# Kernel optimization log

Measured on AMD Instinct MI355X. Metric: run time of the kernel, lower is better.

Reference implementation:

```python
import jax, jax.numpy as jnp
import numpy as np

N_NODES = 100000
N_EDGES = 600000
D = 128


def setup_inputs() -> dict:
    key = jax.random.key(0)
    k_h, k_ei, k_ea, k_wm, k_bm, k_wu, k_bu = jax.random.split(key, 7)
    h = jax.random.normal(k_h, (N_NODES, D), dtype=jnp.float32)
    edge_index = jax.random.randint(k_ei, (2, N_EDGES), 0, N_NODES, dtype=jnp.int64)
    edge_attr = jax.random.normal(k_ea, (N_EDGES, D), dtype=jnp.float32)
    # nn.Linear params (W stored as [out, in] in torch; keep [in, out] here)
    s_m = 1.0 / np.sqrt(3 * D)
    s_u = 1.0 / np.sqrt(2 * D)
    W_msg = jax.random.uniform(k_wm, (3 * D, D), jnp.float32, -s_m, s_m)
    b_msg = jax.random.uniform(k_bm, (D,), jnp.float32, -s_m, s_m)
    W_upd = jax.random.uniform(k_wu, (2 * D, D), jnp.float32, -s_u, s_u)
    b_upd = jax.random.uniform(k_bu, (D,), jnp.float32, -s_u, s_u)
    return {"h": h, "edge_index": edge_index, "edge_attr": edge_attr,
            "W_msg": W_msg, "b_msg": b_msg, "W_upd": W_upd, "b_upd": b_upd}


def reference(h, edge_index, edge_attr, W_msg, b_msg, W_upd, b_upd):
    send, rec = edge_index[0], edge_index[1]
    h_send = h[send]                      # [E, D] gather
    h_rec = h[rec]                        # [E, D] gather
    msg_in = jnp.concatenate((h_send, h_rec, edge_attr), axis=1)  # [E, 3D]
    messages = msg_in @ W_msg + b_msg     # [E, D]
    messages_agg = jax.ops.segment_sum(messages, rec, num_segments=h.shape[0])  # [N, D]
    upd_in = jnp.concatenate((h, messages_agg), axis=1)           # [N, 2D]
    out = upd_in @ W_upd + b_upd          # [N, D]
    return out
```

## Files before the change

### kernel.cpp

```cpp
#include <hip/hip_runtime.h>

#define N_NODES 100000
#define N_EDGES 600000
#define D 128
#define MAXDEG 64
#define OVF_CAP 4096

typedef __attribute__((ext_vector_type(8))) short bf16x8;
typedef __attribute__((ext_vector_type(4))) float f32x4;

static __device__ inline ushort f2bf(float f) {
    unsigned x = __float_as_uint(f);
    unsigned r = (x + 0x7fffu + ((x >> 16) & 1u)) >> 16;
    return (ushort)r;
}


__global__ void k_zero(int* __restrict__ cnt) {
    int i = blockIdx.x * 256 + threadIdx.x;
    if (i < N_NODES + 1) cnt[i] = 0;
}

__global__ void k_build_w(const float* __restrict__ W_msg,
                          const float* __restrict__ b_msg,
                          const float* __restrict__ W_upd,
                          ushort* __restrict__ Wfrag,
                          float* __restrict__ Wcat32,
                          float* __restrict__ bv)
{
    int gid = blockIdx.x * 256 + threadIdx.x;
    if (gid < 512 * 128) {
        int i = gid & 7;
        int l = (gid >> 3) & 63;
        int fb = gid >> 9;
        int kb = fb >> 3, cb = fb & 7;
        int k = kb * 32 + ((l >> 4) * 8) + i;
        int j = cb * 16 + (l & 15);
        float acc;
        if (k < 128) {
            acc = W_upd[k * 128 + j];
        } else {
            int r = k - 128;
            acc = 0.f;
            #pragma unroll 4
            for (int dd = 0; dd < 128; ++dd)
                acc += W_msg[r * 128 + dd] * W_upd[(128 + dd) * 128 + j];
        }
        Wfrag[gid] = f2bf(acc);
        Wcat32[k * 128 + j] = acc;
    } else if (gid < 512 * 128 + 128) {
        int j = gid - 512 * 128;
        float acc = 0.f;
        for (int dd = 0; dd < 128; ++dd)
            acc += b_msg[dd] * W_upd[(128 + dd) * 128 + j];
        bv[j] = acc;
    }
}

__global__ void k_bucket(const int* __restrict__ eidx,
                         int* __restrict__ cnt,
                         int* __restrict__ ovf,
                         int2* __restrict__ elist2)
{
    int e = blockIdx.x * 256 + threadIdx.x;
    if (e >= N_EDGES) return;
    int s = eidx[e];
    int r = eidx[N_EDGES + e];
    int slot = atomicAdd(cnt + r, 1);
    if (slot < MAXDEG) {
        elist2[(size_t)r * MAXDEG + slot] = make_int2(e, s);
    } else {
        int p = atomicAdd(cnt + N_NODES, 1);
        if (p < OVF_CAP) ovf[p] = e;
    }
}

__global__ __launch_bounds__(256, 4) void k_fused(
    const float* __restrict__ h,
    const float* __restrict__ ea,
    const int* __restrict__ cnt,
    const int2* __restrict__ elist2,
    const ushort* __restrict__ Wfrag,
    const float* __restrict__ bv,
    const float* __restrict__ b_upd,
    float* __restrict__ out)
{
    __shared__ ushort Xs[32][520];
    __shared__ float degL[32];
    const int tid = threadIdx.x;
    const int lane = tid & 63;
    const int wv = tid >> 6;
    const int n0 = blockIdx.x * 32;

    for (int u = 0; u < 8; ++u) {
        const int i = wv * 8 + u;
        const int n = n0 + i;
        const int c = cnt[n];
        const int m = c < MAXDEG ? c : MAXDEG;
        const float2 hn = *(const float2*)(h + (size_t)n * D + lane * 2);
        int2 es = make_int2(0, 0);
        if (lane < m) es = elist2[(size_t)n * MAXDEG + lane];

        float Sx = 0.f, Sy = 0.f, Ex = 0.f, Ey = 0.f;
        int t = 0;
        for (; t + 4 <= m; t += 4) {
            int e0 = __shfl(es.x, t + 0), s0 = __shfl(es.y, t + 0);
            int e1 = __shfl(es.x, t + 1), s1 = __shfl(es.y, t + 1);
            int e2 = __shfl(es.x, t + 2), s2 = __shfl(es.y, t + 2);
            int e3 = __shfl(es.x, t + 3), s3 = __shfl(es.y, t + 3);
            float2 a0 = *(const float2*)(h  + (size_t)s0 * D + lane * 2);
            float2 a1 = *(const float2*)(h  + (size_t)s1 * D + lane * 2);
            float2 a2 = *(const float2*)(h  + (size_t)s2 * D + lane * 2);
            float2 a3 = *(const float2*)(h  + (size_t)s3 * D + lane * 2);
            float2 b0 = *(const float2*)(ea + (size_t)e0 * D + lane * 2);
            float2 b1 = *(const float2*)(ea + (size_t)e1 * D + lane * 2);
            float2 b2 = *(const float2*)(ea + (size_t)e2 * D + lane * 2);
            float2 b3 = *(const float2*)(ea + (size_t)e3 * D + lane * 2);
            Sx += (a0.x + a1.x) + (a2.x + a3.x);
            Sy += (a0.y + a1.y) + (a2.y + a3.y);
            Ex += (b0.x + b1.x) + (b2.x + b3.x);
            Ey += (b0.y + b1.y) + (b2.y + b3.y);
        }
        for (; t < m; ++t) {
            int e = __shfl(es.x, t), s = __shfl(es.y, t);
            float2 a = *(const float2*)(h  + (size_t)s * D + lane * 2);
            float2 b = *(const float2*)(ea + (size_t)e * D + lane * 2);
            Sx += a.x; Sy += a.y; Ex += b.x; Ey += b.y;
        }
        const float dv = (float)c;
        ushort2 q;
        q.x = f2bf(hn.x);      q.y = f2bf(hn.y);
        *(ushort2*)&Xs[i][      lane * 2] = q;
        q.x = f2bf(Sx);        q.y = f2bf(Sy);
        *(ushort2*)&Xs[i][128 + lane * 2] = q;
        q.x = f2bf(dv * hn.x); q.y = f2bf(dv * hn.y);
        *(ushort2*)&Xs[i][256 + lane * 2] = q;
        q.x = f2bf(Ex);        q.y = f2bf(Ey);
        *(ushort2*)&Xs[i][384 + lane * 2] = q;
        if (lane == 0) degL[i] = dv;
    }
    __syncthreads();

    const int rb = wv >> 1;
    const int cbg = wv & 1;
    const int arow = rb * 16 + (lane & 15);
    const int koff = (lane >> 4) * 8;

    f32x4 acc[4] = {};
    for (int kb = 0; kb < 16; ++kb) {
        bf16x8 a = *(const bf16x8*)&Xs[arow][kb * 32 + koff];
        #pragma unroll
        for (int cc = 0; cc < 4; ++cc) {
            int fb = kb * 8 + cbg * 4 + cc;
            bf16x8 b = *(const bf16x8*)(Wfrag + ((size_t)fb * 64 + lane) * 8);
            acc[cc] = __builtin_amdgcn_mfma_f32_16x16x32_bf16(a, b, acc[cc], 0, 0, 0);
        }
    }

    const int r0 = (lane >> 4) * 4;
    #pragma unroll
    for (int cc = 0; cc < 4; ++cc) {
        int col = cbg * 64 + cc * 16 + (lane & 15);
        float bvv = bv[col];
        float buv = b_upd[col];
        #pragma unroll
        for (int r = 0; r < 4; ++r) {
            int rl = rb * 16 + r0 + r;
            out[(size_t)(n0 + rl) * D + col] = acc[cc][r] + degL[rl] * bvv + buv;
        }
    }
}

__global__ void k_ovf(const float* __restrict__ h,
                      const int* __restrict__ eidx,
                      const float* __restrict__ ea,
                      const int* __restrict__ cnt,
                      const int* __restrict__ ovf,
                      const float* __restrict__ Wcat32,
                      float* __restrict__ out)
{
    int ncnt = cnt[N_NODES];
    if (ncnt > OVF_CAP) ncnt = OVF_CAP;
    if (ncnt <= 0) return;
    int lane = threadIdx.x & 63;
    int w = threadIdx.x >> 6;
    for (int i = w; i < ncnt; i += 4) {
        int e = ovf[i];
        int s = eidx[e];
        int r = eidx[N_EDGES + e];
        float acc0 = 0.f, acc1 = 0.f;
        for (int dd = 0; dd < 128; ++dd) {
            float hs = h[(size_t)s * D + dd];
            float ev = ea[(size_t)e * D + dd];
            acc0 += hs * Wcat32[(128 + dd) * 128 + lane * 2]     + ev * Wcat32[(384 + dd) * 128 + lane * 2];
            acc1 += hs * Wcat32[(128 + dd) * 128 + lane * 2 + 1] + ev * Wcat32[(384 + dd) * 128 + lane * 2 + 1];
        }
        atomicAdd(out + (size_t)r * D + lane * 2 + 0, acc0);
        atomicAdd(out + (size_t)r * D + lane * 2 + 1, acc1);
    }
}

extern "C" void kernel_launch(void* const* d_in, const int* in_sizes, int n_in,
                              void* d_out, int out_size, void* d_ws, size_t ws_size,
                              hipStream_t stream)
{
    const float* h     = (const float*)d_in[0];
    const int*   eidx  = (const int*)d_in[1];
    const float* eattr = (const float*)d_in[2];
    const float* W_msg = (const float*)d_in[3];
    const float* b_msg = (const float*)d_in[4];
    const float* W_upd = (const float*)d_in[5];
    const float* b_upd = (const float*)d_in[6];
    float* out = (float*)d_out;

    ushort* Wfrag  = (ushort*)d_ws;
    float*  Wcat32 = (float*)((char*)d_ws + 131072);
    float*  bv     = Wcat32 + 512 * 128;
    int*    cnt    = (int*)(bv + 128);
    int*    ovf    = cnt + 100002;
    int2*   elist2 = (int2*)(ovf + OVF_CAP);

    k_zero<<<(N_NODES + 1 + 255) / 256, 256, 0, stream>>>(cnt);
    k_build_w<<<(512 * 128 + 128 + 255) / 256, 256, 0, stream>>>(W_msg, b_msg, W_upd, Wfrag, Wcat32, bv);
    k_bucket<<<(N_EDGES + 255) / 256, 256, 0, stream>>>(eidx, cnt, ovf, elist2);
    k_fused<<<N_NODES / 32, 256, 0, stream>>>(h, eattr, cnt, elist2, Wfrag, bv, b_upd, out);
    k_ovf<<<1, 256, 0, stream>>>(h, eidx, eattr, cnt, ovf, Wcat32, out);
}
```

Before: 201.1 us.

## Shrink node tile to 16, prefetch next node's edge list, stream edge_attr nontemporally

The fused gather+MFMA kernel now processes 16 nodes per block instead of 32, which doubles the grid and raises the launch-bounds occupancy hint to 8 blocks per CU. Each wave software-prefetches the next node's edge list, degree and h row while reducing the current node. Edge_attr rows are read with nontemporal loads to keep them from displacing h in cache. The MFMA phase is re-split so each wave computes 32 output columns of the 16-row tile, which means each block reloads the full weight fragments for half as many rows.

```diff
diff --git a/kernel.cpp b/kernel.cpp
--- a/kernel.cpp
+++ b/kernel.cpp
@@ -5,14 +5,20 @@
 #define D 128
 #define MAXDEG 64
 #define OVF_CAP 4096
+#define BM 16
 
 typedef __attribute__((ext_vector_type(8))) short bf16x8;
 typedef __attribute__((ext_vector_type(4))) float f32x4;
+typedef __attribute__((ext_vector_type(2))) float f32x2;
 
 static __device__ inline ushort f2bf(float f) {
     unsigned x = __float_as_uint(f);
     unsigned r = (x + 0x7fffu + ((x >> 16) & 1u)) >> 16;
     return (ushort)r;
+}
+
+static __device__ inline f32x2 nt_load2(const float* p) {
+    return __builtin_nontemporal_load((const f32x2*)p);
 }
 
 
@@ -75,7 +81,7 @@
     }
 }
 
-__global__ __launch_bounds__(256, 4) void k_fused(
+__global__ __launch_bounds__(256, 8) void k_fused(
     const float* __restrict__ h,
     const float* __restrict__ ea,
     const int* __restrict__ cnt,
@@ -85,21 +91,28 @@
     const float* __restrict__ b_upd,
     float* __restrict__ out)
 {
-    __shared__ ushort Xs[32][520];
-    __shared__ float degL[32];
+    __shared__ ushort Xs[BM][520];
+    __shared__ float degL[BM];
     const int tid = threadIdx.x;
     const int lane = tid & 63;
     const int wv = tid >> 6;
-    const int n0 = blockIdx.x * 32;
-
-    for (int u = 0; u < 8; ++u) {
-        const int i = wv * 8 + u;
-        const int n = n0 + i;
-        const int c = cnt[n];
+    const int n0 = blockIdx.x * BM;
+    const int nb = n0 + wv * 4;
+
+    int2 es = elist2[(size_t)nb * MAXDEG + lane];
+    int   c = cnt[nb];
+    f32x2 hn = *(const f32x2*)(h + (size_t)nb * D + lane * 2);
+
+    for (int u = 0; u < 4; ++u) {
+        const int i = wv * 4 + u;
+        const int n = nb + u;
+        int2 es_n; int c_n; f32x2 hn_n;
+        if (u < 3) {
+            es_n = elist2[(size_t)(n + 1) * MAXDEG + lane];
+            c_n  = cnt[n + 1];
+            hn_n = *(const f32x2*)(h + (size_t)(n + 1) * D + lane * 2);
+        }
         const int m = c < MAXDEG ? c : MAXDEG;
-        const float2 hn = *(const float2*)(h + (size_t)n * D + lane * 2);
-        int2 es = make_int2(0, 0);
-        if (lane < m) es = elist2[(size_t)n * MAXDEG + lane];
 
         float Sx = 0.f, Sy = 0.f, Ex = 0.f, Ey = 0.f;
         int t = 0;
@@ -108,50 +121,49 @@
             int e1 = __shfl(es.x, t + 1), s1 = __shfl(es.y, t + 1);
             int e2 = __shfl(es.x, t + 2), s2 = __shfl(es.y, t + 2);
             int e3 = __shfl(es.x, t + 3), s3 = __shfl(es.y, t + 3);
-            float2 a0 = *(const float2*)(h  + (size_t)s0 * D + lane * 2);
-            float2 a1 = *(const float2*)(h  + (size_t)s1 * D + lane * 2);
-            float2 a2 = *(const float2*)(h  + (size_t)s2 * D + lane * 2);
-            float2 a3 = *(const float2*)(h  + (size_t)s3 * D + lane * 2);
-            float2 b0 = *(const float2*)(ea + (size_t)e0 * D + lane * 2);
-            float2 b1 = *(const float2*)(ea + (size_t)e1 * D + lane * 2);
-            float2 b2 = *(const float2*)(ea + (size_t)e2 * D + lane * 2);
-            float2 b3 = *(const float2*)(ea + (size_t)e3 * D + lane * 2);
-            Sx += (a0.x + a1.x) + (a2.x + a3.x);
-            Sy += (a0.y + a1.y) + (a2.y + a3.y);
-            Ex += (b0.x + b1.x) + (b2.x + b3.x);
-            Ey += (b0.y + b1.y) + (b2.y + b3.y);
+            f32x2 a0 = *(const f32x2*)(h + (size_t)s0 * D + lane * 2);
+            f32x2 a1 = *(const f32x2*)(h + (size_t)s1 * D + lane * 2);
+            f32x2 a2 = *(const f32x2*)(h + (size_t)s2 * D + lane * 2);
+            f32x2 a3 = *(const f32x2*)(h + (size_t)s3 * D + lane * 2);
+            f32x2 b0 = nt_load2(ea + (size_t)e0 * D + lane * 2);
+            f32x2 b1 = nt_load2(ea + (size_t)e1 * D + lane * 2);
+            f32x2 b2 = nt_load2(ea + (size_t)e2 * D + lane * 2);
+            f32x2 b3 = nt_load2(ea + (size_t)e3 * D + lane * 2);
+            Sx += (a0[0] + a1[0]) + (a2[0] + a3[0]);
+            Sy += (a0[1] + a1[1]) + (a2[1] + a3[1]);
+            Ex += (b0[0] + b1[0]) + (b2[0] + b3[0]);
+            Ey += (b0[1] + b1[1]) + (b2[1] + b3[1]);
         }
         for (; t < m; ++t) {
             int e = __shfl(es.x, t), s = __shfl(es.y, t);
-            float2 a = *(const float2*)(h  + (size_t)s * D + lane * 2);
-            float2 b = *(const float2*)(ea + (size_t)e * D + lane * 2);
-            Sx += a.x; Sy += a.y; Ex += b.x; Ey += b.y;
+            f32x2 a = *(const f32x2*)(h + (size_t)s * D + lane * 2);
+            f32x2 b = nt_load2(ea + (size_t)e * D + lane * 2);
+            Sx += a[0]; Sy += a[1]; Ex += b[0]; Ey += b[1];
         }
         const float dv = (float)c;
         ushort2 q;
-        q.x = f2bf(hn.x);      q.y = f2bf(hn.y);
+        q.x = f2bf(hn[0]);      q.y = f2bf(hn[1]);
         *(ushort2*)&Xs[i][      lane * 2] = q;
-        q.x = f2bf(Sx);        q.y = f2bf(Sy);
+        q.x = f2bf(Sx);         q.y = f2bf(Sy);
         *(ushort2*)&Xs[i][128 + lane * 2] = q;
-        q.x = f2bf(dv * hn.x); q.y = f2bf(dv * hn.y);
+        q.x = f2bf(dv * hn[0]); q.y = f2bf(dv * hn[1]);
         *(ushort2*)&Xs[i][256 + lane * 2] = q;
-        q.x = f2bf(Ex);        q.y = f2bf(Ey);
+        q.x = f2bf(Ex);         q.y = f2bf(Ey);
         *(ushort2*)&Xs[i][384 + lane * 2] = q;
         if (lane == 0) degL[i] = dv;
+        es = es_n; c = c_n; hn = hn_n;
     }
     __syncthreads();
 
-    const int rb = wv >> 1;
-    const int cbg = wv & 1;
-    const int arow = rb * 16 + (lane & 15);
+    const int arow = lane & 15;
     const int koff = (lane >> 4) * 8;
 
-    f32x4 acc[4] = {};
+    f32x4 acc[2] = {};
     for (int kb = 0; kb < 16; ++kb) {
         bf16x8 a = *(const bf16x8*)&Xs[arow][kb * 32 + koff];
         #pragma unroll
-        for (int cc = 0; cc < 4; ++cc) {
-            int fb = kb * 8 + cbg * 4 + cc;
+        for (int cc = 0; cc < 2; ++cc) {
+            int fb = kb * 8 + wv * 2 + cc;
             bf16x8 b = *(const bf16x8*)(Wfrag + ((size_t)fb * 64 + lane) * 8);
             acc[cc] = __builtin_amdgcn_mfma_f32_16x16x32_bf16(a, b, acc[cc], 0, 0, 0);
         }
@@ -159,13 +171,13 @@
 
     const int r0 = (lane >> 4) * 4;
     #pragma unroll
-    for (int cc = 0; cc < 4; ++cc) {
-        int col = cbg * 64 + cc * 16 + (lane & 15);
+    for (int cc = 0; cc < 2; ++cc) {
+        int col = wv * 32 + cc * 16 + (lane & 15);
         float bvv = bv[col];
         float buv = b_upd[col];
         #pragma unroll
         for (int r = 0; r < 4; ++r) {
-            int rl = rb * 16 + r0 + r;
+            int rl = r0 + r;
             out[(size_t)(n0 + rl) * D + col] = acc[cc][r] + degL[rl] * bvv + buv;
         }
     }
@@ -223,6 +235,6 @@
     k_zero<<<(N_NODES + 1 + 255) / 256, 256, 0, stream>>>(cnt);
     k_build_w<<<(512 * 128 + 128 + 255) / 256, 256, 0, stream>>>(W_msg, b_msg, W_upd, Wfrag, Wcat32, bv);
     k_bucket<<<(N_EDGES + 255) / 256, 256, 0, stream>>>(eidx, cnt, ovf, elist2);
-    k_fused<<<N_NODES / 32, 256, 0, stream>>>(h, eattr, cnt, elist2, Wfrag, bv, b_upd, out);
+    k_fused<<<N_NODES / BM, 256, 0, stream>>>(h, eattr, cnt, elist2, Wfrag, bv, b_upd, out);
     k_ovf<<<1, 256, 0, stream>>>(h, eidx, eattr, cnt, ovf, Wcat32, out);
 }
```

New measurement: 175.9 us. -12.5%, faster.

## Split fused gather+GEMM, gather bf16 node features, nontemporal edge loads

Applied to the files above, without the earlier changes.

Adds a pre-pass that converts h to bf16 so the random neighbor gathers move half the bytes. The fused kernel is split into a high-occupancy gather kernel, which writes per-node bf16 neighbor sums, edge sums and degree to workspace, and a separate MFMA GEMM kernel that reads those rows back. Edge attributes are read with nontemporal loads so they do not evict the gathered h rows from cache. The cost is an extra full pass over h, an extra intermediate write and read, two more launches, and reduced precision in the neighbor sums.

```diff
diff --git a/kernel.cpp b/kernel.cpp
--- a/kernel.cpp
+++ b/kernel.cpp
@@ -5,14 +5,26 @@
 #define D 128
 #define MAXDEG 64
 #define OVF_CAP 4096
+#define BM 32
 
 typedef __attribute__((ext_vector_type(8))) short bf16x8;
 typedef __attribute__((ext_vector_type(4))) float f32x4;
+typedef __attribute__((ext_vector_type(2))) float f32x2;
 
 static __device__ inline ushort f2bf(float f) {
     unsigned x = __float_as_uint(f);
     unsigned r = (x + 0x7fffu + ((x >> 16) & 1u)) >> 16;
     return (ushort)r;
+}
+static __device__ inline float bf2f(ushort u) {
+    return __uint_as_float((unsigned)u << 16);
+}
+static __device__ inline f32x2 nt_load2(const float* p) {
+    return __builtin_nontemporal_load((const f32x2*)p);
+}
+static __device__ inline unsigned mulpack2(unsigned a, float dv) {
+    return (unsigned)f2bf(dv * bf2f((ushort)a)) |
+           ((unsigned)f2bf(dv * bf2f((ushort)(a >> 16))) << 16);
 }
 
 
@@ -57,6 +69,15 @@
     }
 }
 
+__global__ void k_hcvt(const float* __restrict__ h, ushort* __restrict__ h16) {
+    int gid = blockIdx.x * 256 + threadIdx.x;
+    if (gid >= N_NODES * D / 4) return;
+    f32x4 v = *(const f32x4*)(h + (size_t)gid * 4);
+    ushort4 u;
+    u.x = f2bf(v[0]); u.y = f2bf(v[1]); u.z = f2bf(v[2]); u.w = f2bf(v[3]);
+    *(ushort4*)(h16 + (size_t)gid * 4) = u;
+}
+
 __global__ void k_bucket(const int* __restrict__ eidx,
                          int* __restrict__ cnt,
                          int* __restrict__ ovf,
@@ -75,72 +96,96 @@
     }
 }
 
-__global__ __launch_bounds__(256, 4) void k_fused(
-    const float* __restrict__ h,
+__global__ __launch_bounds__(256, 8) void k_gather2(
+    const ushort* __restrict__ h16,
     const float* __restrict__ ea,
     const int* __restrict__ cnt,
     const int2* __restrict__ elist2,
+    ushort* __restrict__ Sea16,
+    float* __restrict__ deg)
+{
+    int gid = blockIdx.x * 256 + threadIdx.x;
+    int n = gid >> 6;
+    int lane = gid & 63;
+    if (n >= N_NODES) return;
+    const int c = cnt[n];
+    const int m = c < MAXDEG ? c : MAXDEG;
+    int2 es = make_int2(0, 0);
+    if (lane < m) es = elist2[(size_t)n * MAXDEG + lane];
+
+    float Sx = 0.f, Sy = 0.f, Ex = 0.f, Ey = 0.f;
+    int t = 0;
+    for (; t + 4 <= m; t += 4) {
+        int e0 = __shfl(es.x, t + 0), s0 = __shfl(es.y, t + 0);
+        int e1 = __shfl(es.x, t + 1), s1 = __shfl(es.y, t + 1);
+        int e2 = __shfl(es.x, t + 2), s2 = __shfl(es.y, t + 2);
+        int e3 = __shfl(es.x, t + 3), s3 = __shfl(es.y, t + 3);
+        unsigned a0 = *(const unsigned*)(h16 + (size_t)s0 * D + lane * 2);
+        unsigned a1 = *(const unsigned*)(h16 + (size_t)s1 * D + lane * 2);
+        unsigned a2 = *(const unsigned*)(h16 + (size_t)s2 * D + lane * 2);
+        unsigned a3 = *(const unsigned*)(h16 + (size_t)s3 * D + lane * 2);
+        f32x2 b0 = nt_load2(ea + (size_t)e0 * D + lane * 2);
+        f32x2 b1 = nt_load2(ea + (size_t)e1 * D + lane * 2);
+        f32x2 b2 = nt_load2(ea + (size_t)e2 * D + lane * 2);
+        f32x2 b3 = nt_load2(ea + (size_t)e3 * D + lane * 2);
+        Sx += (bf2f((ushort)a0) + bf2f((ushort)a1)) + (bf2f((ushort)a2) + bf2f((ushort)a3));
+        Sy += (bf2f((ushort)(a0 >> 16)) + bf2f((ushort)(a1 >> 16))) +
+              (bf2f((ushort)(a2 >> 16)) + bf2f((ushort)(a3 >> 16)));
+        Ex += (b0[0] + b1[0]) + (b2[0] + b3[0]);
+        Ey += (b0[1] + b1[1]) + (b2[1] + b3[1]);
+    }
+    for (; t < m; ++t) {
+        int e = __shfl(es.x, t), s = __shfl(es.y, t);
+        unsigned a = *(const unsigned*)(h16 + (size_t)s * D + lane * 2);
+        f32x2 b = nt_load2(ea + (size_t)e * D + lane * 2);
+        Sx += bf2f((ushort)a); Sy += bf2f((ushort)(a >> 16));
+        Ex += b[0]; Ey += b[1];
+    }
+
+    unsigned sp = (unsigned)f2bf(Sx) | ((unsigned)f2bf(Sy) << 16);
+    unsigned ep = (unsigned)f2bf(Ex) | ((unsigned)f2bf(Ey) << 16);
+    *(unsigned*)(Sea16 + (size_t)n * 256 + lane * 2) = sp;
+    *(unsigned*)(Sea16 + (size_t)n * 256 + 128 + lane * 2) = ep;
+    if (lane == 0) deg[n] = (float)c;
+}
+
+__global__ __launch_bounds__(256, 4) void k_gemm(
+    const ushort* __restrict__ h16,
+    const ushort* __restrict__ Sea16,
+    const float* __restrict__ deg,
     const ushort* __restrict__ Wfrag,
     const float* __restrict__ bv,
     const float* __restrict__ b_upd,
     float* __restrict__ out)
 {
-    __shared__ ushort Xs[32][520];
-    __shared__ float degL[32];
+    __shared__ ushort Xs[BM][520];
+    __shared__ float degL[BM];
     const int tid = threadIdx.x;
+    const int n0 = blockIdx.x * BM;
+    if (tid < BM) degL[tid] = deg[n0 + tid];
+
+    for (int q = tid; q < BM * 64; q += 256) {
+        int i = q >> 6, j = q & 63;
+        int n = n0 + i;
+        uint4 v;
+        if (j < 16) {
+            v = *(const uint4*)(h16 + (size_t)n * D + j * 8);
+        } else if (j < 32) {
+            v = *(const uint4*)(Sea16 + (size_t)n * 256 + (j - 16) * 8);
+        } else if (j < 48) {
+            uint4 a = *(const uint4*)(h16 + (size_t)n * D + (j - 32) * 8);
+            float dv = deg[n];
+            v.x = mulpack2(a.x, dv); v.y = mulpack2(a.y, dv);
+            v.z = mulpack2(a.z, dv); v.w = mulpack2(a.w, dv);
+        } else {
+            v = *(const uint4*)(Sea16 + (size_t)n * 256 + 128 + (j - 48) * 8);
+        }
+        *(uint4*)&Xs[i][j * 8] = v;
+    }
+    __syncthreads();
+
     const int lane = tid & 63;
     const int wv = tid >> 6;
-    const int n0 = blockIdx.x * 32;
-
-    for (int u = 0; u < 8; ++u) {
-        const int i = wv * 8 + u;
-        const int n = n0 + i;
-        const int c = cnt[n];
-        const int m = c < MAXDEG ? c : MAXDEG;
-        const float2 hn = *(const float2*)(h + (size_t)n * D + lane * 2);
-        int2 es = make_int2(0, 0);
-        if (lane < m) es = elist2[(size_t)n * MAXDEG + lane];
-
-        float Sx = 0.f, Sy = 0.f, Ex = 0.f, Ey = 0.f;
-        int t = 0;
-        for (; t + 4 <= m; t += 4) {
-            int e0 = __shfl(es.x, t + 0), s0 = __shfl(es.y, t + 0);
-            int e1 = __shfl(es.x, t + 1), s1 = __shfl(es.y, t + 1);
-            int e2 = __shfl(es.x, t + 2), s2 = __shfl(es.y, t + 2);
-            int e3 = __shfl(es.x, t + 3), s3 = __shfl(es.y, t + 3);
-            float2 a0 = *(const float2*)(h  + (size_t)s0 * D + lane * 2);
-            float2 a1 = *(const float2*)(h  + (size_t)s1 * D + lane * 2);
-            float2 a2 = *(const float2*)(h  + (size_t)s2 * D + lane * 2);
-            float2 a3 = *(const float2*)(h  + (size_t)s3 * D + lane * 2);
-            float2 b0 = *(const float2*)(ea + (size_t)e0 * D + lane * 2);
-            float2 b1 = *(const float2*)(ea + (size_t)e1 * D + lane * 2);
-            float2 b2 = *(const float2*)(ea + (size_t)e2 * D + lane * 2);
-            float2 b3 = *(const float2*)(ea + (size_t)e3 * D + lane * 2);
-            Sx += (a0.x + a1.x) + (a2.x + a3.x);
-            Sy += (a0.y + a1.y) + (a2.y + a3.y);
-            Ex += (b0.x + b1.x) + (b2.x + b3.x);
-            Ey += (b0.y + b1.y) + (b2.y + b3.y);
-        }
-        for (; t < m; ++t) {
-            int e = __shfl(es.x, t), s = __shfl(es.y, t);
-            float2 a = *(const float2*)(h  + (size_t)s * D + lane * 2);
-            float2 b = *(const float2*)(ea + (size_t)e * D + lane * 2);
-            Sx += a.x; Sy += a.y; Ex += b.x; Ey += b.y;
-        }
-        const float dv = (float)c;
-        ushort2 q;
-        q.x = f2bf(hn.x);      q.y = f2bf(hn.y);
-        *(ushort2*)&Xs[i][      lane * 2] = q;
-        q.x = f2bf(Sx);        q.y = f2bf(Sy);
-        *(ushort2*)&Xs[i][128 + lane * 2] = q;
-        q.x = f2bf(dv * hn.x); q.y = f2bf(dv * hn.y);
-        *(ushort2*)&Xs[i][256 + lane * 2] = q;
-        q.x = f2bf(Ex);        q.y = f2bf(Ey);
-        *(ushort2*)&Xs[i][384 + lane * 2] = q;
-        if (lane == 0) degL[i] = dv;
-    }
-    __syncthreads();
-
     const int rb = wv >> 1;
     const int cbg = wv & 1;
     const int arow = rb * 16 + (lane & 15);
@@ -213,16 +258,22 @@
     const float* b_upd = (const float*)d_in[6];
     float* out = (float*)d_out;
 
-    ushort* Wfrag  = (ushort*)d_ws;
-    float*  Wcat32 = (float*)((char*)d_ws + 131072);
-    float*  bv     = Wcat32 + 512 * 128;
-    int*    cnt    = (int*)(bv + 128);
-    int*    ovf    = cnt + 100002;
-    int2*   elist2 = (int2*)(ovf + OVF_CAP);
+    char* base = (char*)d_ws;
+    ushort* Wfrag  = (ushort*)(base);
+    float*  Wcat32 = (float*)(base + 131072);
+    float*  bv     = (float*)(base + 393216);
+    float*  deg    = (float*)(base + 393728);
+    int*    cnt    = (int*)(base + 793728);
+    int*    ovf    = (int*)(base + 1193984);
+    int2*   elist2 = (int2*)(base + 1210368);
+    ushort* h16    = (ushort*)(base + 52410368);
+    ushort* Sea16  = (ushort*)(base + 78010368);
 
     k_zero<<<(N_NODES + 1 + 255) / 256, 256, 0, stream>>>(cnt);
     k_build_w<<<(512 * 128 + 128 + 255) / 256, 256, 0, stream>>>(W_msg, b_msg, W_upd, Wfrag, Wcat32, bv);
+    k_hcvt<<<(N_NODES * D / 4 + 255) / 256, 256, 0, stream>>>(h, h16);
     k_bucket<<<(N_EDGES + 255) / 256, 256, 0, stream>>>(eidx, cnt, ovf, elist2);
-    k_fused<<<N_NODES / 32, 256, 0, stream>>>(h, eattr, cnt, elist2, Wfrag, bv, b_upd, out);
+    k_gather2<<<(N_NODES * 64 + 255) / 256, 256, 0, stream>>>(h16, eattr, cnt, elist2, Sea16, deg);
+    k_gemm<<<N_NODES / BM, 256, 0, stream>>>(h16, Sea16, deg, Wfrag, bv, b_upd, out);
     k_ovf<<<1, 256, 0, stream>>>(h, eidx, eattr, cnt, ovf, Wcat32, out);
 }
```

Result: no change. 202.8 us (+0.9%).
